# Kernel optimization log

Measured on AMD Instinct MI355X. Metric: run time of the kernel, lower is better.

## Reference

```python
import jax, jax.numpy as jnp
import numpy as np

NUM_HEADS = 8  # must match init num_heads
EPS = 1e-12    # torch F.normalize eps


def _conv2d(x, w, pad, groups=1):
    # x: NCHW, w: OIHW
    return jax.lax.conv_general_dilated(
        x, w, window_strides=(1, 1), padding=[(pad, pad), (pad, pad)],
        feature_group_count=groups,
        dimension_numbers=('NCHW', 'OIHW', 'NCHW'))


def _cmul(a, b):
    # complex multiply on trailing dim of size 2 (re, im)
    re = a[..., 0] * b[..., 0] - a[..., 1] * b[..., 1]
    im = a[..., 0] * b[..., 1] + a[..., 1] * b[..., 0]
    return jnp.stack([re, im], axis=-1)


def setup_inputs() -> dict:
    key = jax.random.key(0)
    ks = jax.random.split(key, 7)
    B, coils, H, W = 8, 16, 384, 384
    C2 = 192
    x = jax.random.normal(ks[0], (B, 2 * coils, H, W), jnp.float32)
    e = jax.random.normal(ks[1], (B, 1, H, W), jnp.float32)
    sens_map = jax.random.normal(ks[2], (B, coils, H, W, 2), jnp.float32)
    # imhead: 1x1 conv (2 -> 2*C2) then depthwise 3x3 (groups = 2*C2), bias-free
    w_im1 = jax.random.normal(ks[3], (2 * C2, 2, 1, 1), jnp.float32) * 0.5
    w_im2 = jax.random.normal(ks[4], (2 * C2, 1, 3, 3), jnp.float32) * 0.2
    # ehead: full 3x3 conv (1 -> C2), bias-free
    w_e = jax.random.normal(ks[5], (C2, 1, 3, 3), jnp.float32) * 0.2
    # project_out: 1x1 conv (C2 -> 2), bias=False
    w_proj = jax.random.normal(ks[6], (2, C2, 1, 1), jnp.float32) * 0.1
    a1 = jnp.ones((NUM_HEADS, 1, 1), jnp.float32)
    return {'x': x, 'e': e, 'sens_map': sens_map,
            'w_im1': w_im1, 'w_im2': w_im2, 'w_e': w_e,
            'w_proj': w_proj, 'a1': a1}


def reference(x, e, sens_map, w_im1, w_im2, w_e, w_proj, a1):
    B, C, H, W = x.shape
    # --- reduce_operator: coil combine ---
    xc = x.reshape(B, -1, H, W, 2)                       # (B, coils, H, W, 2)
    sens_conj = jnp.stack([sens_map[..., 0], -sens_map[..., 1]], axis=-1)
    red = _cmul(xc, sens_conj).sum(axis=1)               # (B, H, W, 2)
    ximg = jnp.transpose(red, (0, 3, 1, 2))              # (B, 2, H, W)
    # --- heads ---
    q1 = _conv2d(ximg, w_im1, pad=0)                     # (B, 2*C2, H, W)
    q1 = _conv2d(q1, w_im2, pad=1, groups=q1.shape[1])   # depthwise 3x3
    k_eg = _conv2d(e, w_e, pad=1)                        # (B, C2, H, W)
    C2 = k_eg.shape[1]
    q_im, v_im = q1[:, :C2], q1[:, C2:]
    h = NUM_HEADS
    c = C2 // h
    n = H * W
    q = q_im.reshape(B, h, c, n)
    k = k_eg.reshape(B, h, c, n)
    v = v_im.reshape(B, h, c, n)
    # L2-normalize over the (large) spatial dim
    q = q / jnp.maximum(jnp.linalg.norm(q, axis=-1, keepdims=True), EPS)
    k = k / jnp.maximum(jnp.linalg.norm(k, axis=-1, keepdims=True), EPS)
    attn = jnp.einsum('bhcn,bhdn->bhcd', q, k) * a1      # (B, h, c, c)
    attn = jax.nn.softmax(attn, axis=-1)
    out = jnp.einsum('bhcd,bhdn->bhcn', attn, v)         # (B, h, c, n)
    out = out.reshape(B, C2, H, W)
    out = _conv2d(out, w_proj, pad=0)                    # (B, 2, H, W)
    out = ximg + out
    out = jnp.transpose(out, (0, 2, 3, 1))               # (B, H, W, 2)
    # --- expand_operator: back to multicoil ---
    xout = _cmul(out[:, None], sens_map)                 # (B, coils, H, W, 2)
    return xout.reshape(B, -1, H, W)                     # (B, 2*coils, H, W)
```

## Files before the change

### kernel.cpp

```cpp
#include <hip/hip_runtime.h>
#include <math.h>

#define B_     8
#define NCOIL  16
#define H_     384
#define W_     384
#define HW     (H_*W_)
#define STRIPS 16
#define ROWS_PER (H_/STRIPS)

#define WS_CACC 0
#define WS_G    3888
#define WS_XIMG 4224

__global__ void ka_coil_reduce(const float* __restrict__ x,
                               const float* __restrict__ sens,
                               float* __restrict__ ws) {
    int b = blockIdx.y;
    int t = blockIdx.x * blockDim.x + threadIdx.x;
    if (blockIdx.x == 0) {
        for (int i = threadIdx.x; i < 6*81; i += blockDim.x)
            ws[WS_CACC + b*6*81 + i] = 0.f;
    }
    if (t >= HW/2) return;
    const float4* xp = (const float4*)(x    + (size_t)b*NCOIL*HW*2);
    const float4* sp = (const float4*)(sens + (size_t)b*NCOIL*HW*2);
    float re0=0.f, im0=0.f, re1=0.f, im1=0.f;
    #pragma unroll 4
    for (int c = 0; c < NCOIL; ++c) {
        float4 xv = xp[(size_t)c*(HW/2) + t];
        float4 sv = sp[(size_t)c*(HW/2) + t];
        re0 += xv.x*sv.x + xv.y*sv.y;
        im0 += xv.y*sv.x - xv.x*sv.y;
        re1 += xv.z*sv.z + xv.w*sv.w;
        im1 += xv.w*sv.z - xv.z*sv.w;
    }
    float* x0 = ws + WS_XIMG + ((size_t)b*2+0)*HW;
    float* x1 = ws + WS_XIMG + ((size_t)b*2+1)*HW;
    ((float2*)x0)[t] = make_float2(re0, re1);
    ((float2*)x1)[t] = make_float2(im0, im1);
}

__global__ __launch_bounds__(W_) void kb_corr(const float* __restrict__ e,
                                              const float* __restrict__ ws_r,
                                              float* __restrict__ ws) {
    const int c = threadIdx.x;
    const int strip = blockIdx.x;
    const int pair = blockIdx.y;
    const int b = blockIdx.z;
    const float* imgs[3];
    imgs[0] = ws_r + WS_XIMG + ((size_t)b*2+0)*HW;
    imgs[1] = ws_r + WS_XIMG + ((size_t)b*2+1)*HW;
    imgs[2] = e + (size_t)b*HW;
    const int pa[6] = {0,1,0,0,1,2};
    const int pb[6] = {2,2,0,1,1,2};
    const float* A  = imgs[pa[pair]];
    const float* Bm = imgs[pb[pair]];

    __shared__ float lA[3][W_+2];
    __shared__ float lB[3][W_+2];
    if (c == 0) {
        #pragma unroll
        for (int s=0;s<3;s++){ lA[s][0]=0.f; lA[s][W_+1]=0.f; lB[s][0]=0.f; lB[s][W_+1]=0.f; }
    }
    float acc[9][9];
    #pragma unroll
    for (int i=0;i<9;i++)
        #pragma unroll
        for (int j=0;j<9;j++) acc[i][j]=0.f;

    const int r0 = strip * ROWS_PER;
    {
        int rr = r0 - 1;
        int slot = (r0 + 2) % 3;
        lA[slot][c+1] = (rr >= 0) ? A [rr*W_ + c] : 0.f;
        lB[slot][c+1] = (rr >= 0) ? Bm[rr*W_ + c] : 0.f;
        rr = r0; slot = r0 % 3;
        lA[slot][c+1] = A [rr*W_ + c];
        lB[slot][c+1] = Bm[rr*W_ + c];
    }
    for (int r = r0; r < r0 + ROWS_PER; ++r) {
        __syncthreads();
        int rr = r + 1;
        int slot = rr % 3;
        lA[slot][c+1] = (rr < H_) ? A [rr*W_ + c] : 0.f;
        lB[slot][c+1] = (rr < H_) ? Bm[rr*W_ + c] : 0.f;
        __syncthreads();
        float aw[3][3], bw[3][3];
        #pragma unroll
        for (int i=0;i<3;i++){
            int s = (r - 1 + i + 3) % 3;
            #pragma unroll
            for (int k=0;k<3;k++){
                aw[i][k] = lA[s][c+k];
                bw[i][k] = lB[s][c+k];
            }
        }
        #pragma unroll
        for (int i=0;i<9;i++)
            #pragma unroll
            for (int j=0;j<9;j++)
                acc[i][j] += aw[i/3][i%3] * bw[j/3][j%3];
    }
    float* dst = ws + WS_CACC + ((size_t)(b*6 + pair))*81;
    #pragma unroll
    for (int i=0;i<9;i++)
        #pragma unroll
        for (int j=0;j<9;j++) {
            float v = acc[i][j];
            #pragma unroll
            for (int off=32; off>0; off>>=1) v += __shfl_down(v, off, 64);
            if ((threadIdx.x & 63) == 0)
                atomicAdd(dst + i*9 + j, v);
        }
}

__global__ void kc_attn(const float* __restrict__ w_im1,
                        const float* __restrict__ w_im2,
                        const float* __restrict__ w_e,
                        const float* __restrict__ w_proj,
                        const float* __restrict__ a1,
                        float* __restrict__ ws) {
    const int b = blockIdx.x;
    const int tid = threadIdx.x;
    const float* C   = ws + WS_CACC + (size_t)b*6*81;
    const float* D0  = C;
    const float* D1  = C + 81;
    const float* E00 = C + 162;
    const float* E01 = C + 243;
    const float* E11 = C + 324;
    const float* F   = C + 405;

    __shared__ float nk[192];
    __shared__ float P[192][24];
    __shared__ float Wm[2][192];

    float tmp1[9];
    float nq = 0.f;
    if (tid < 192) {
        const int j = tid;
        float Aq0[9], Aq1[9];
        const float w0 = w_im1[j*2+0], w1 = w_im1[j*2+1];
        #pragma unroll
        for (int t=0;t<9;t++){ float w2 = w_im2[j*9+t]; Aq0[t]=w0*w2; Aq1[t]=w1*w2; }
        #pragma unroll
        for (int u=0;u<9;u++){
            float s = 0.f;
            #pragma unroll
            for (int t=0;t<9;t++) s += Aq0[t]*D0[t*9+u] + Aq1[t]*D1[t*9+u];
            tmp1[u] = s;
        }
        float nq2 = 0.f;
        #pragma unroll
        for (int t=0;t<9;t++)
            #pragma unroll
            for (int u=0;u<9;u++)
                nq2 += Aq0[t]*Aq0[u]*E00[t*9+u] + Aq1[t]*Aq1[u]*E11[t*9+u]
                     + Aq0[t]*Aq1[u]*E01[t*9+u] + Aq1[t]*Aq0[u]*E01[u*9+t];
        nq = sqrtf(fmaxf(nq2, 0.f));
        float nk2 = 0.f;
        #pragma unroll
        for (int t=0;t<9;t++)
            #pragma unroll
            for (int u=0;u<9;u++)
                nk2 += w_e[j*9+t]*w_e[j*9+u]*F[t*9+u];
        nk[j] = sqrtf(fmaxf(nk2, 0.f));
    }
    __syncthreads();
    if (tid < 192) {
        const int j = tid, h = j/24;
        const float a1h = a1[h];
        const float inq = 1.f / fmaxf(nq, 1e-12f);
        float l[24]; float m = -1e30f;
        #pragma unroll
        for (int d=0; d<24; ++d) {
            const float* we = w_e + (h*24+d)*9;
            float s = 0.f;
            #pragma unroll
            for (int u=0;u<9;u++) s += tmp1[u]*we[u];
            s = s * a1h * inq / fmaxf(nk[h*24+d], 1e-12f);
            l[d] = s; m = fmaxf(m, s);
        }
        float sum = 0.f;
        #pragma unroll
        for (int d=0;d<24;d++){ float p = __expf(l[d]-m); l[d]=p; sum+=p; }
        const float isum = 1.f/sum;
        #pragma unroll
        for (int d=0;d<24;d++) P[j][d] = l[d]*isum;
    }
    __syncthreads();
    if (tid < 384) {
        const int pch = tid/192, xx = tid%192, h = xx/24, d = xx%24;
        float s = 0.f;
        #pragma unroll
        for (int c=0;c<24;c++) s += w_proj[pch*192 + h*24 + c] * P[h*24+c][d];
        Wm[pch][xx] = s;
    }
    __syncthreads();
    if (tid < 36) {
        const int pch = tid/18, rem = tid%18, r = rem/9, t9 = rem%9;
        float s = 0.f;
        for (int j=0;j<192;j++)
            s += Wm[pch][j] * w_im1[(192+j)*2 + r] * w_im2[(192+j)*9 + t9];
        ws[WS_G + b*36 + pch*18 + r*9 + t9] = s;
    }
}

__global__ void kd_out(const float* __restrict__ sens,
                       const float* __restrict__ ws,
                       float* __restrict__ out) {
    const int b = blockIdx.y;
    const int t = blockIdx.x*blockDim.x + threadIdx.x;
    if (t >= HW/2) return;
    const int p0 = 2*t;
    const int row = p0 / W_, col = p0 % W_;
    const float* gm = ws + WS_G + b*36;
    const float* X0 = ws + WS_XIMG + ((size_t)b*2+0)*HW;
    const float* X1 = ws + WS_XIMG + ((size_t)b*2+1)*HW;

    float n0[3][4], n1[3][4];
    #pragma unroll
    for (int i=0;i<3;i++){
        const int rr = row-1+i;
        const bool rok = (rr>=0 && rr<H_);
        #pragma unroll
        for (int k=0;k<4;k++){
            const int cc = col-1+k;
            const bool ok = rok && (cc>=0) && (cc<W_);
            n0[i][k] = ok ? X0[rr*W_+cc] : 0.f;
            n1[i][k] = ok ? X1[rr*W_+cc] : 0.f;
        }
    }
    float ore[2], oim[2];
    #pragma unroll
    for (int px=0; px<2; ++px) {
        float a0 = n0[1][1+px];
        float a1v = n1[1][1+px];
        #pragma unroll
        for (int i=0;i<3;i++)
            #pragma unroll
            for (int k=0;k<3;k++){
                const float v0 = n0[i][k+px], v1 = n1[i][k+px];
                a0  += gm[ 0 + i*3+k]*v0 + gm[ 9 + i*3+k]*v1;
                a1v += gm[18 + i*3+k]*v0 + gm[27 + i*3+k]*v1;
            }
        ore[px] = a0; oim[px] = a1v;
    }
    const float4* sp = (const float4*)(sens + (size_t)b*NCOIL*HW*2);
    float4* op = (float4*)(out + (size_t)b*NCOIL*HW*2);
    for (int c=0;c<NCOIL;c++){
        float4 sv = sp[(size_t)c*(HW/2)+t];
        float4 ov;
        ov.x = ore[0]*sv.x - oim[0]*sv.y;
        ov.y = ore[0]*sv.y + oim[0]*sv.x;
        ov.z = ore[1]*sv.z - oim[1]*sv.w;
        ov.w = ore[1]*sv.w + oim[1]*sv.z;
        op[(size_t)c*(HW/2)+t] = ov;
    }
}

extern "C" void kernel_launch(void* const* d_in, const int* in_sizes, int n_in,
                              void* d_out, int out_size, void* d_ws, size_t ws_size,
                              hipStream_t stream) {
    const float* x      = (const float*)d_in[0];
    const float* e      = (const float*)d_in[1];
    const float* sens   = (const float*)d_in[2];
    const float* w_im1  = (const float*)d_in[3];
    const float* w_im2  = (const float*)d_in[4];
    const float* w_e    = (const float*)d_in[5];
    const float* w_proj = (const float*)d_in[6];
    const float* a1     = (const float*)d_in[7];
    float* ws  = (float*)d_ws;
    float* out = (float*)d_out;

    dim3 gA(HW/2/256, B_);
    ka_coil_reduce<<<gA, 256, 0, stream>>>(x, sens, ws);
    dim3 gB(STRIPS, 6, B_);
    kb_corr<<<gB, W_, 0, stream>>>(e, ws, ws);
    kc_attn<<<dim3(B_), 384, 0, stream>>>(w_im1, w_im2, w_e, w_proj, a1, ws);
    dim3 gD(HW/2/256, B_);
    kd_out<<<gD, 256, 0, stream>>>(sens, ws, out);
}
```

Before: 571.7 us.

## Register-tile kb_corr: 6 columns x 6 rows per thread, drop shared-memory row buffers

```diff
diff --git a/kernel.cpp b/kernel.cpp
--- a/kernel.cpp
+++ b/kernel.cpp
@@ -6,8 +6,10 @@
 #define H_     384
 #define W_     384
 #define HW     (H_*W_)
-#define STRIPS 16
-#define ROWS_PER (H_/STRIPS)
+
+#define KB_STRIPS 16
+#define KB_TC     6
+#define KB_RPT    6
 
 #define WS_CACC 0
 #define WS_G    3888
@@ -41,78 +43,86 @@
     ((float2*)x1)[t] = make_float2(im0, im1);
 }
 
-__global__ __launch_bounds__(W_) void kb_corr(const float* __restrict__ e,
-                                              const float* __restrict__ ws_r,
-                                              float* __restrict__ ws) {
-    const int c = threadIdx.x;
-    const int strip = blockIdx.x;
+__device__ __forceinline__ void kb_load_row(const float* __restrict__ img,
+                                            int r, int c0, float* dst) {
+    if (r < 0 || r >= H_) {
+        #pragma unroll
+        for (int k = 0; k < KB_TC+2; ++k) dst[k] = 0.f;
+        return;
+    }
+    const float* p = img + r*W_ + (c0 - 1);
+    #pragma unroll
+    for (int k = 0; k < KB_TC+2; ++k) {
+        const int cc = c0 - 1 + k;
+        dst[k] = (cc >= 0 && cc < W_) ? p[k] : 0.f;
+    }
+}
+
+__global__ __launch_bounds__(256) void kb_corr(const float* __restrict__ e,
+                                               const float* __restrict__ ws_r,
+                                               float* __restrict__ ws) {
+    const int tid  = threadIdx.x;
+    const int cg   = tid & 63;
+    const int rg   = tid >> 6;
+    const int strip= blockIdx.x;
     const int pair = blockIdx.y;
-    const int b = blockIdx.z;
+    const int b    = blockIdx.z;
+
     const float* imgs[3];
     imgs[0] = ws_r + WS_XIMG + ((size_t)b*2+0)*HW;
     imgs[1] = ws_r + WS_XIMG + ((size_t)b*2+1)*HW;
     imgs[2] = e + (size_t)b*HW;
     const int pa[6] = {0,1,0,0,1,2};
     const int pb[6] = {2,2,0,1,1,2};
-    const float* A  = imgs[pa[pair]];
-    const float* Bm = imgs[pb[pair]];
-
-    __shared__ float lA[3][W_+2];
-    __shared__ float lB[3][W_+2];
-    if (c == 0) {
-        #pragma unroll
-        for (int s=0;s<3;s++){ lA[s][0]=0.f; lA[s][W_+1]=0.f; lB[s][0]=0.f; lB[s][W_+1]=0.f; }
-    }
-    float acc[9][9];
-    #pragma unroll
-    for (int i=0;i<9;i++)
-        #pragma unroll
-        for (int j=0;j<9;j++) acc[i][j]=0.f;
-
-    const int r0 = strip * ROWS_PER;
-    {
-        int rr = r0 - 1;
-        int slot = (r0 + 2) % 3;
-        lA[slot][c+1] = (rr >= 0) ? A [rr*W_ + c] : 0.f;
-        lB[slot][c+1] = (rr >= 0) ? Bm[rr*W_ + c] : 0.f;
-        rr = r0; slot = r0 % 3;
-        lA[slot][c+1] = A [rr*W_ + c];
-        lB[slot][c+1] = Bm[rr*W_ + c];
-    }
-    for (int r = r0; r < r0 + ROWS_PER; ++r) {
-        __syncthreads();
-        int rr = r + 1;
-        int slot = rr % 3;
-        lA[slot][c+1] = (rr < H_) ? A [rr*W_ + c] : 0.f;
-        lB[slot][c+1] = (rr < H_) ? Bm[rr*W_ + c] : 0.f;
-        __syncthreads();
-        float aw[3][3], bw[3][3];
-        #pragma unroll
-        for (int i=0;i<3;i++){
-            int s = (r - 1 + i + 3) % 3;
-            #pragma unroll
-            for (int k=0;k<3;k++){
-                aw[i][k] = lA[s][c+k];
-                bw[i][k] = lB[s][c+k];
+    const float* __restrict__ A  = imgs[pa[pair]];
+    const float* __restrict__ Bm = imgs[pb[pair]];
+
+    const int c0      = cg * KB_TC;
+    const int r_start = strip * (KB_RPT*4) + rg * KB_RPT;
+
+    float acc[81];
+    #pragma unroll
+    for (int i = 0; i < 81; ++i) acc[i] = 0.f;
+
+    float wA[3][KB_TC+2], wB[3][KB_TC+2];
+    kb_load_row(A,  r_start-1, c0, wA[0]);
+    kb_load_row(Bm, r_start-1, c0, wB[0]);
+    kb_load_row(A,  r_start,   c0, wA[1]);
+    kb_load_row(Bm, r_start,   c0, wB[1]);
+
+    for (int r = r_start; r < r_start + KB_RPT; ++r) {
+        kb_load_row(A,  r+1, c0, wA[2]);
+        kb_load_row(Bm, r+1, c0, wB[2]);
+        #pragma unroll
+        for (int m = 0; m < KB_TC; ++m) {
+            #pragma unroll
+            for (int t = 0; t < 9; ++t) {
+                const float av = wA[t/3][m + t%3];
+                #pragma unroll
+                for (int u = 0; u < 9; ++u)
+                    acc[t*9+u] += av * wB[u/3][m + u%3];
             }
         }
         #pragma unroll
-        for (int i=0;i<9;i++)
-            #pragma unroll
-            for (int j=0;j<9;j++)
-                acc[i][j] += aw[i/3][i%3] * bw[j/3][j%3];
-    }
-    float* dst = ws + WS_CACC + ((size_t)(b*6 + pair))*81;
-    #pragma unroll
-    for (int i=0;i<9;i++)
-        #pragma unroll
-        for (int j=0;j<9;j++) {
-            float v = acc[i][j];
-            #pragma unroll
-            for (int off=32; off>0; off>>=1) v += __shfl_down(v, off, 64);
-            if ((threadIdx.x & 63) == 0)
-                atomicAdd(dst + i*9 + j, v);
-        }
+        for (int k = 0; k < KB_TC+2; ++k) {
+            wA[0][k] = wA[1][k]; wA[1][k] = wA[2][k];
+            wB[0][k] = wB[1][k]; wB[1][k] = wB[2][k];
+        }
+    }
+
+    __shared__ float red[4][81];
+    #pragma unroll
+    for (int i = 0; i < 81; ++i) {
+        float v = acc[i];
+        v += __shfl_xor(v, 1);  v += __shfl_xor(v, 2);  v += __shfl_xor(v, 4);
+        v += __shfl_xor(v, 8);  v += __shfl_xor(v, 16); v += __shfl_xor(v, 32);
+        if (cg == 0) red[rg][i] = v;
+    }
+    __syncthreads();
+    if (tid < 81) {
+        float* dst = ws + WS_CACC + ((size_t)(b*6 + pair))*81;
+        atomicAdd(dst + tid, red[0][tid] + red[1][tid] + red[2][tid] + red[3][tid]);
+    }
 }
 
 __global__ void kc_attn(const float* __restrict__ w_im1,
@@ -275,8 +285,8 @@
 
     dim3 gA(HW/2/256, B_);
     ka_coil_reduce<<<gA, 256, 0, stream>>>(x, sens, ws);
-    dim3 gB(STRIPS, 6, B_);
-    kb_corr<<<gB, W_, 0, stream>>>(e, ws, ws);
+    dim3 gB(KB_STRIPS, 6, B_);
+    kb_corr<<<gB, 256, 0, stream>>>(e, ws, ws);
     kc_attn<<<dim3(B_), 384, 0, stream>>>(w_im1, w_im2, w_e, w_proj, a1, ws);
     dim3 gD(HW/2/256, B_);
     kd_out<<<gD, 256, 0, stream>>>(sens, ws, out);
```

After: 473.4 us. 1.21x faster.
